# Kernel optimization log

Measured on AMD Instinct MI355X. Metric: run time of the kernel, lower is better.

Reference implementation:

```python
import jax, jax.numpy as jnp
import numpy as np

N, K, V_FEATS, FILTERS = 50000, 20, 128, 128


def setup_inputs() -> dict:
    key = jax.random.key(0)
    ks = jax.random.split(key, 10)
    vertices = jax.random.normal(ks[0], (N, V_FEATS), dtype=jnp.float32)
    nh_indices = jax.random.randint(ks[1], (N, K), -1, N, dtype=jnp.int32)
    int_indices = jax.random.randint(ks[2], (N, K), -1, N, dtype=jnp.int32)
    nh_edges = jax.random.uniform(ks[3], (N, K), dtype=jnp.float32)
    int_edges = jax.random.uniform(ks[4], (N, K), dtype=jnp.float32)
    is_int = jax.random.randint(ks[5], (N,), 0, 2, dtype=jnp.int32)
    scale = 1.0 / np.sqrt(V_FEATS)
    Wvc = jax.random.normal(ks[6], (V_FEATS, FILTERS), dtype=jnp.float32) * scale
    Wvn_int = jax.random.normal(ks[7], (V_FEATS, FILTERS), dtype=jnp.float32) * scale
    Wvn_nh = jax.random.normal(ks[8], (V_FEATS, FILTERS), dtype=jnp.float32) * scale
    bv = jnp.zeros((FILTERS,), dtype=jnp.float32)
    return {"vertices": vertices, "nh_indices": nh_indices, "int_indices": int_indices,
            "nh_edges": nh_edges, "int_edges": int_edges, "is_int": is_int,
            "Wvc": Wvc, "Wvn_int": Wvn_int, "Wvn_nh": Wvn_nh, "bv": bv}


def _gather_agg(v_proj, indices, edges):
    # v_proj: [N, F]; indices: [N, K] (-1 = pad); edges: [N, K]
    mask = (indices != -1)[..., None].astype(v_proj.dtype)            # [N, K, 1]
    norm = jnp.maximum(jnp.sum(indices > -1, axis=1, keepdims=True), 1).astype(v_proj.dtype)  # [N, 1]
    safe_idx = jnp.where(indices < 0, 0, indices)                      # masked slots -> dummy row 0
    gathered = v_proj[safe_idx]                                        # [N, K, F]
    return jnp.sum(gathered * mask * edges[..., None], axis=1) / norm  # [N, F]


def reference(vertices, nh_indices, int_indices, nh_edges, int_edges, is_int,
              Wvc, Wvn_int, Wvn_nh, bv):
    Zc = vertices @ Wvc                                # [N, F]
    v_Wvn_int = vertices @ Wvn_int                     # [N, F]
    v_Wvn_nh = vertices @ Wvn_nh                       # [N, F]
    Zn_inter = _gather_agg(v_Wvn_int, int_indices, int_edges)
    Zn_nh = _gather_agg(v_Wvn_nh, nh_indices, nh_edges)
    z = jax.nn.relu(Zc + Zn_inter + Zn_nh + bv)        # bias=True; dropout omitted (eval)
    return (z, nh_indices, int_indices, nh_edges, int_edges, is_int)
```

## Files before the change

### kernel.cpp

```cpp
#include <hip/hip_runtime.h>

#define N_VERT 50000
#define KNBR 20
#define F 128
#define NBLK 782

typedef unsigned int uint32;
typedef unsigned short ushort16;
typedef unsigned char uint8;
typedef __attribute__((ext_vector_type(8))) short bf16x8;
typedef __attribute__((ext_vector_type(4))) float f32x4;

__device__ __forceinline__ uint32 f2bf_bits(float x) {
    uint32 u = __float_as_uint(x);
    u += 0x7fff + ((u >> 16) & 1);
    return u >> 16;
}

__global__ __launch_bounds__(256) void wconv_kernel(
    const float* __restrict__ Wc, const float* __restrict__ Wi,
    const float* __restrict__ Wn, const float* __restrict__ bv,
    ushort16* __restrict__ Wt, float* __restrict__ bvp)
{
    int t = blockIdx.x * 256 + threadIdx.x;
    if (blockIdx.x == 0 && threadIdx.x < 128) {
        int c = threadIdx.x;
        bvp[c] = bv[(c & 7) * 16 + (c >> 3)];
    }
    if (t >= 3 * F * F) return;
    int w    = t >> 14;
    int r    = t & 16383;
    int kk   = r >> 12;
    int r2   = r & 4095;
    int nt   = r2 >> 9;
    int r3   = r2 & 511;
    int lane = r3 >> 3;
    int e    = r3 & 7;
    int k = kk * 32 + (lane >> 4) * 8 + e;
    int n = nt * 16 + (lane & 15);
    const float* W = (w == 0) ? Wc : ((w == 1) ? Wi : Wn);
    Wt[t] = (ushort16)f2bf_bits(W[k * F + n]);
}

__global__ __launch_bounds__(256) void mfma_proj_kernel(
    const float*    __restrict__ vert,
    const ushort16* __restrict__ Wt,
    const float*    __restrict__ bvp,
    ushort16* __restrict__ zcp,
    uint8* __restrict__ pay_i, float* __restrict__ sc_i,
    uint8* __restrict__ pay_n, float* __restrict__ sc_n)
{
    const int w    = blockIdx.y;
    const int wave = threadIdx.x >> 6;
    const int lane = threadIdx.x & 63;
    const int lr   = lane & 15;
    const int lk   = lane >> 4;
    const int rb   = (blockIdx.x * 4 + wave) * 16;

    int rowA = rb + lr; if (rowA > N_VERT - 1) rowA = N_VERT - 1;
    const float* vrow = vert + (size_t)rowA * F;
    bf16x8 afrag[4];
#pragma unroll
    for (int kk = 0; kk < 4; ++kk) {
        const float* p = vrow + kk * 32 + lk * 8;
        f32x4 lo = *(const f32x4*)p;
        f32x4 hi = *(const f32x4*)(p + 4);
#pragma unroll
        for (int j = 0; j < 4; ++j) {
            afrag[kk][j]     = (short)f2bf_bits(lo[j]);
            afrag[kk][4 + j] = (short)f2bf_bits(hi[j]);
        }
    }

    f32x4 acc[8];
#pragma unroll
    for (int nt = 0; nt < 8; ++nt) acc[nt] = (f32x4)(0.f);

#pragma unroll
    for (int kk = 0; kk < 4; ++kk)
#pragma unroll
        for (int nt = 0; nt < 8; ++nt) {
            bf16x8 b = *(const bf16x8*)(
                Wt + ((size_t)((w * 4 + kk) * 8 + nt)) * 512 + lane * 8);
            acc[nt] = __builtin_amdgcn_mfma_f32_16x16x32_bf16(
                afrag[kk], b, acc[nt], 0, 0, 0);
        }

    if (w == 0) {
        f32x4 bb0 = *(const f32x4*)(bvp + lr * 8);
        f32x4 bb1 = *(const f32x4*)(bvp + lr * 8 + 4);
        float bbv[8] = {bb0[0], bb0[1], bb0[2], bb0[3], bb1[0], bb1[1], bb1[2], bb1[3]};
#pragma unroll
        for (int j = 0; j < 4; ++j) {
            int row = rb + lk * 4 + j;
            uint32 d[4];
#pragma unroll
            for (int p = 0; p < 4; ++p)
                d[p] = f2bf_bits(acc[2 * p][j] + bbv[2 * p]) |
                       (f2bf_bits(acc[2 * p + 1][j] + bbv[2 * p + 1]) << 16);
            if (row < N_VERT)
                *(uint4*)((uint8*)zcp + (size_t)row * 256 + lr * 16) =
                    make_uint4(d[0], d[1], d[2], d[3]);
        }
    } else {
        uint8* pay = (w == 1) ? pay_i : pay_n;
        float* sc  = (w == 1) ? sc_i : sc_n;
        float m0 = 0.f, m1 = 0.f, m2 = 0.f, m3 = 0.f;
#pragma unroll
        for (int nt = 0; nt < 8; ++nt) {
            m0 = fmaxf(m0, fabsf(acc[nt][0]));
            m1 = fmaxf(m1, fabsf(acc[nt][1]));
            m2 = fmaxf(m2, fabsf(acc[nt][2]));
            m3 = fmaxf(m3, fabsf(acc[nt][3]));
        }
#pragma unroll
        for (int s = 1; s < 16; s <<= 1) {
            m0 = fmaxf(m0, __shfl_xor(m0, s));
            m1 = fmaxf(m1, __shfl_xor(m1, s));
            m2 = fmaxf(m2, __shfl_xor(m2, s));
            m3 = fmaxf(m3, __shfl_xor(m3, s));
        }
        float mj[4] = {m0, m1, m2, m3};
#pragma unroll
        for (int j = 0; j < 4; ++j) {
            int row = rb + lk * 4 + j;
            float inv = (mj[j] > 0.f) ? 127.f / mj[j] : 0.f;
            uint32 lo = 0, hi = 0;
#pragma unroll
            for (int nt = 0; nt < 4; ++nt) {
                int q0 = (int)rintf(acc[nt][j] * inv);
                int q1 = (int)rintf(acc[nt + 4][j] * inv);
                lo |= ((uint32)(q0 & 255)) << (8 * nt);
                hi |= ((uint32)(q1 & 255)) << (8 * nt);
            }
            if (row < N_VERT)
                *(uint2*)(pay + (size_t)row * 128 + lr * 8) = make_uint2(lo, hi);
        }
        float s_sel = (lr == 0) ? m0 : (lr == 1) ? m1 : (lr == 2) ? m2 : m3;
        if (lr < 4) {
            int row = rb + lk * 4 + lr;
            if (row < N_VERT) sc[row] = s_sel * (1.f / 127.f);
        }
    }
}

__global__ __launch_bounds__(256) void agg_kernel(
    const uint8*  __restrict__ pay_i, const float* __restrict__ sc_i,
    const uint8*  __restrict__ pay_n, const float* __restrict__ sc_n,
    const unsigned short* __restrict__ zcp,
    const int4*   __restrict__ int_idx4,
    const int4*   __restrict__ nh_idx4,
    const float4* __restrict__ int_e4,
    const float4* __restrict__ nh_e4,
    float* __restrict__ z)
{
    const int lane = threadIdx.x & 63;
    const int wave = threadIdx.x >> 6;
    const int vg   = lane >> 4;
    const int fg   = lane & 15;
    const int i    = blockIdx.x * 16 + wave * 4 + vg;

    float a_i[8], a_n[8];
#pragma unroll
    for (int j = 0; j < 8; ++j) { a_i[j] = 0.f; a_n[j] = 0.f; }
    int ci = 0, cn = 0;

    {
        int sidx[KNBR]; float f[KNBR];
#pragma unroll
        for (int q = 0; q < 5; ++q) {
            int4   a = int_idx4[i * 5 + q];
            float4 e = int_e4[i * 5 + q];
            int   av[4] = {a.x, a.y, a.z, a.w};
            float ev[4] = {e.x, e.y, e.z, e.w};
#pragma unroll
            for (int j = 0; j < 4; ++j) {
                bool v = av[j] >= 0;
                ci += v;
                sidx[4 * q + j] = v ? av[j] : 0;
                f[4 * q + j]    = v ? ev[j] : 0.f;
            }
        }
#pragma unroll
        for (int k = 0; k < KNBR; ++k) f[k] *= sc_i[sidx[k]];
        uint2 g[KNBR];
#pragma unroll
        for (int k = 0; k < KNBR; ++k)
            g[k] = *(const uint2*)(pay_i + (size_t)sidx[k] * 128 + fg * 8);
#pragma unroll
        for (int k = 0; k < KNBR; ++k) {
            float e = f[k];
            uint32 d0 = g[k].x, d1 = g[k].y;
#pragma unroll
            for (int b = 0; b < 4; ++b) {
                a_i[b]     = fmaf((float)((int)(d0 << (24 - 8 * b)) >> 24), e, a_i[b]);
                a_i[4 + b] = fmaf((float)((int)(d1 << (24 - 8 * b)) >> 24), e, a_i[4 + b]);
            }
        }
    }
    {
        int sidx[KNBR]; float f[KNBR];
#pragma unroll
        for (int q = 0; q < 5; ++q) {
            int4   a = nh_idx4[i * 5 + q];
            float4 e = nh_e4[i * 5 + q];
            int   av[4] = {a.x, a.y, a.z, a.w};
            float ev[4] = {e.x, e.y, e.z, e.w};
#pragma unroll
            for (int j = 0; j < 4; ++j) {
                bool v = av[j] >= 0;
                cn += v;
                sidx[4 * q + j] = v ? av[j] : 0;
                f[4 * q + j]    = v ? ev[j] : 0.f;
            }
        }
#pragma unroll
        for (int k = 0; k < KNBR; ++k) f[k] *= sc_n[sidx[k]];
        uint2 g[KNBR];
#pragma unroll
        for (int k = 0; k < KNBR; ++k)
            g[k] = *(const uint2*)(pay_n + (size_t)sidx[k] * 128 + fg * 8);
#pragma unroll
        for (int k = 0; k < KNBR; ++k) {
            float e = f[k];
            uint32 d0 = g[k].x, d1 = g[k].y;
#pragma unroll
            for (int b = 0; b < 4; ++b) {
                a_n[b]     = fmaf((float)((int)(d0 << (24 - 8 * b)) >> 24), e, a_n[b]);
                a_n[4 + b] = fmaf((float)((int)(d1 << (24 - 8 * b)) >> 24), e, a_n[4 + b]);
            }
        }
    }

    float ri = 1.f / (float)max(ci, 1);
    float rn = 1.f / (float)max(cn, 1);

    uint4 zq = *(const uint4*)(zcp + (size_t)i * 128 + fg * 8);
    uint32 zd[4] = {zq.x, zq.y, zq.z, zq.w};
    float* zrow = z + (size_t)i * F + fg;
#pragma unroll
    for (int t = 0; t < 8; ++t) {
        uint32 dw = zd[t >> 1];
        float zc = __uint_as_float((t & 1) ? (dw & 0xffff0000u) : (dw << 16));
        float r  = zc + a_i[t] * ri + a_n[t] * rn;
        zrow[t * 16] = fmaxf(r, 0.f);
    }
}

__global__ void pass_kernel(const int*   __restrict__ nh_idx,
                            const int*   __restrict__ int_idx,
                            const float* __restrict__ nh_e,
                            const float* __restrict__ int_e,
                            const int*   __restrict__ is_int,
                            float* __restrict__ out)
{
    const size_t NK    = (size_t)N_VERT * KNBR;
    const size_t total = 4 * NK + N_VERT;
    size_t t = (size_t)blockIdx.x * blockDim.x + threadIdx.x;
    if (t >= total) return;

    float v;
    if      (t <     NK) v = (float)nh_idx[t];
    else if (t < 2 * NK) v = (float)int_idx[t - NK];
    else if (t < 3 * NK) v = nh_e[t - 2 * NK];
    else if (t < 4 * NK) v = int_e[t - 3 * NK];
    else                 v = (float)is_int[t - 4 * NK];
    out[t] = v;
}

extern "C" void kernel_launch(void* const* d_in, const int* in_sizes, int n_in,
                              void* d_out, int out_size, void* d_ws, size_t ws_size,
                              hipStream_t stream) {
    const float* vert    = (const float*)d_in[0];
    const int*   nh_idx  = (const int*)  d_in[1];
    const int*   int_idx = (const int*)  d_in[2];
    const float* nh_e    = (const float*)d_in[3];
    const float* int_e   = (const float*)d_in[4];
    const int*   is_int  = (const int*)  d_in[5];
    const float* Wc      = (const float*)d_in[6];
    const float* Wi      = (const float*)d_in[7];
    const float* Wn      = (const float*)d_in[8];
    const float* bv      = (const float*)d_in[9];

    float* z        = (float*)d_out;
    float* out_rest = z + (size_t)N_VERT * F;

    uint8* pay_i = (uint8*)d_ws;
    uint8* pay_n = pay_i + (size_t)N_VERT * F;
    float* sc_i  = (float*)(pay_n + (size_t)N_VERT * F);
    float* sc_n  = sc_i + N_VERT;
    ushort16* zcp = (ushort16*)(sc_n + N_VERT);
    float* bvp   = (float*)(zcp + (size_t)N_VERT * F);
    ushort16* Wt = (ushort16*)(bvp + F);

    wconv_kernel<<<(3 * F * F + 255) / 256, 256, 0, stream>>>(Wc, Wi, Wn, bv, Wt, bvp);
    mfma_proj_kernel<<<dim3(NBLK, 3), 256, 0, stream>>>(
        vert, Wt, bvp, zcp, pay_i, sc_i, pay_n, sc_n);
    agg_kernel<<<N_VERT / 16, 256, 0, stream>>>(
        pay_i, sc_i, pay_n, sc_n, (const unsigned short*)zcp,
        (const int4*)int_idx, (const int4*)nh_idx,
        (const float4*)int_e, (const float4*)nh_e, z);

    const size_t total = (size_t)4 * N_VERT * KNBR + N_VERT;
    pass_kernel<<<(int)((total + 255) / 256), 256, 0, stream>>>(
        nh_idx, int_idx, nh_e, int_e, is_int, out_rest);
}
```

Measured before the change: 82.92 us.

## Fuse three projections per block and store neighbor payloads as FP8

The projection kernel now computes all three weight projections in one block, so each vertex row is read and converted to bf16 once instead of three times. The int8-with-per-row-scale payload is replaced by hardware FP8 pack/unpack conversions. This drops the max-reduction shuffles, the scale arrays and the per-neighbor scale gathers in the aggregation kernel. The cost is more accumulator registers (three sets of eight) in the projection kernel and lower precision, since FP8 without per-row scaling can lose accuracy or saturate on large values.

```diff
diff --git a/kernel.cpp b/kernel.cpp
--- a/kernel.cpp
+++ b/kernel.cpp
@@ -10,6 +10,7 @@
 typedef unsigned char uint8;
 typedef __attribute__((ext_vector_type(8))) short bf16x8;
 typedef __attribute__((ext_vector_type(4))) float f32x4;
+typedef __attribute__((ext_vector_type(2))) float f32x2;
 
 __device__ __forceinline__ uint32 f2bf_bits(float x) {
     uint32 u = __float_as_uint(x);
@@ -42,15 +43,14 @@
     Wt[t] = (ushort16)f2bf_bits(W[k * F + n]);
 }
 
-__global__ __launch_bounds__(256) void mfma_proj_kernel(
+__global__ __launch_bounds__(256, 3) void mfma_proj_kernel(
     const float*    __restrict__ vert,
     const ushort16* __restrict__ Wt,
     const float*    __restrict__ bvp,
     ushort16* __restrict__ zcp,
-    uint8* __restrict__ pay_i, float* __restrict__ sc_i,
-    uint8* __restrict__ pay_n, float* __restrict__ sc_n)
-{
-    const int w    = blockIdx.y;
+    uint8* __restrict__ pay_i,
+    uint8* __restrict__ pay_n)
+{
     const int wave = threadIdx.x >> 6;
     const int lane = threadIdx.x & 63;
     const int lr   = lane & 15;
@@ -72,81 +72,62 @@
         }
     }
 
-    f32x4 acc[8];
-#pragma unroll
-    for (int nt = 0; nt < 8; ++nt) acc[nt] = (f32x4)(0.f);
+    f32x4 aC[8], aI[8], aN[8];
+#pragma unroll
+    for (int nt = 0; nt < 8; ++nt) {
+        aC[nt] = (f32x4)(0.f); aI[nt] = (f32x4)(0.f); aN[nt] = (f32x4)(0.f);
+    }
 
 #pragma unroll
     for (int kk = 0; kk < 4; ++kk)
 #pragma unroll
         for (int nt = 0; nt < 8; ++nt) {
-            bf16x8 b = *(const bf16x8*)(
-                Wt + ((size_t)((w * 4 + kk) * 8 + nt)) * 512 + lane * 8);
-            acc[nt] = __builtin_amdgcn_mfma_f32_16x16x32_bf16(
-                afrag[kk], b, acc[nt], 0, 0, 0);
-        }
-
-    if (w == 0) {
-        f32x4 bb0 = *(const f32x4*)(bvp + lr * 8);
-        f32x4 bb1 = *(const f32x4*)(bvp + lr * 8 + 4);
-        float bbv[8] = {bb0[0], bb0[1], bb0[2], bb0[3], bb1[0], bb1[1], bb1[2], bb1[3]};
-#pragma unroll
-        for (int j = 0; j < 4; ++j) {
-            int row = rb + lk * 4 + j;
-            uint32 d[4];
-#pragma unroll
-            for (int p = 0; p < 4; ++p)
-                d[p] = f2bf_bits(acc[2 * p][j] + bbv[2 * p]) |
-                       (f2bf_bits(acc[2 * p + 1][j] + bbv[2 * p + 1]) << 16);
-            if (row < N_VERT)
-                *(uint4*)((uint8*)zcp + (size_t)row * 256 + lr * 16) =
-                    make_uint4(d[0], d[1], d[2], d[3]);
-        }
-    } else {
-        uint8* pay = (w == 1) ? pay_i : pay_n;
-        float* sc  = (w == 1) ? sc_i : sc_n;
-        float m0 = 0.f, m1 = 0.f, m2 = 0.f, m3 = 0.f;
-#pragma unroll
-        for (int nt = 0; nt < 8; ++nt) {
-            m0 = fmaxf(m0, fabsf(acc[nt][0]));
-            m1 = fmaxf(m1, fabsf(acc[nt][1]));
-            m2 = fmaxf(m2, fabsf(acc[nt][2]));
-            m3 = fmaxf(m3, fabsf(acc[nt][3]));
-        }
-#pragma unroll
-        for (int s = 1; s < 16; s <<= 1) {
-            m0 = fmaxf(m0, __shfl_xor(m0, s));
-            m1 = fmaxf(m1, __shfl_xor(m1, s));
-            m2 = fmaxf(m2, __shfl_xor(m2, s));
-            m3 = fmaxf(m3, __shfl_xor(m3, s));
-        }
-        float mj[4] = {m0, m1, m2, m3};
-#pragma unroll
-        for (int j = 0; j < 4; ++j) {
-            int row = rb + lk * 4 + j;
-            float inv = (mj[j] > 0.f) ? 127.f / mj[j] : 0.f;
-            uint32 lo = 0, hi = 0;
-#pragma unroll
-            for (int nt = 0; nt < 4; ++nt) {
-                int q0 = (int)rintf(acc[nt][j] * inv);
-                int q1 = (int)rintf(acc[nt + 4][j] * inv);
-                lo |= ((uint32)(q0 & 255)) << (8 * nt);
-                hi |= ((uint32)(q1 & 255)) << (8 * nt);
-            }
-            if (row < N_VERT)
-                *(uint2*)(pay + (size_t)row * 128 + lr * 8) = make_uint2(lo, hi);
-        }
-        float s_sel = (lr == 0) ? m0 : (lr == 1) ? m1 : (lr == 2) ? m2 : m3;
-        if (lr < 4) {
-            int row = rb + lk * 4 + lr;
-            if (row < N_VERT) sc[row] = s_sel * (1.f / 127.f);
-        }
+            const ushort16* base = Wt + (size_t)(kk * 8 + nt) * 512 + lane * 8;
+            bf16x8 bC = *(const bf16x8*)(base);
+            bf16x8 bI = *(const bf16x8*)(base + 32 * 512);
+            bf16x8 bN = *(const bf16x8*)(base + 64 * 512);
+            aC[nt] = __builtin_amdgcn_mfma_f32_16x16x32_bf16(afrag[kk], bC, aC[nt], 0, 0, 0);
+            aI[nt] = __builtin_amdgcn_mfma_f32_16x16x32_bf16(afrag[kk], bI, aI[nt], 0, 0, 0);
+            aN[nt] = __builtin_amdgcn_mfma_f32_16x16x32_bf16(afrag[kk], bN, aN[nt], 0, 0, 0);
+        }
+
+    f32x4 bb0 = *(const f32x4*)(bvp + lr * 8);
+    f32x4 bb1 = *(const f32x4*)(bvp + lr * 8 + 4);
+    float bbv[8] = {bb0[0], bb0[1], bb0[2], bb0[3], bb1[0], bb1[1], bb1[2], bb1[3]};
+#pragma unroll
+    for (int j = 0; j < 4; ++j) {
+        int row = rb + lk * 4 + j;
+        if (row >= N_VERT) continue;
+        uint32 d[4];
+#pragma unroll
+        for (int p = 0; p < 4; ++p)
+            d[p] = f2bf_bits(aC[2 * p][j] + bbv[2 * p]) |
+                   (f2bf_bits(aC[2 * p + 1][j] + bbv[2 * p + 1]) << 16);
+        *(uint4*)((uint8*)zcp + (size_t)row * 256 + lr * 16) =
+            make_uint4(d[0], d[1], d[2], d[3]);
+    }
+
+#pragma unroll
+    for (int j = 0; j < 4; ++j) {
+        int row = rb + lk * 4 + j;
+        if (row >= N_VERT) continue;
+        uint32 lo, hi;
+        lo = __builtin_amdgcn_cvt_pk_fp8_f32(aI[0][j], aI[1][j], 0, false);
+        lo = __builtin_amdgcn_cvt_pk_fp8_f32(aI[2][j], aI[3][j], lo, true);
+        hi = __builtin_amdgcn_cvt_pk_fp8_f32(aI[4][j], aI[5][j], 0, false);
+        hi = __builtin_amdgcn_cvt_pk_fp8_f32(aI[6][j], aI[7][j], hi, true);
+        *(uint2*)(pay_i + (size_t)row * 128 + lr * 8) = make_uint2(lo, hi);
+        lo = __builtin_amdgcn_cvt_pk_fp8_f32(aN[0][j], aN[1][j], 0, false);
+        lo = __builtin_amdgcn_cvt_pk_fp8_f32(aN[2][j], aN[3][j], lo, true);
+        hi = __builtin_amdgcn_cvt_pk_fp8_f32(aN[4][j], aN[5][j], 0, false);
+        hi = __builtin_amdgcn_cvt_pk_fp8_f32(aN[6][j], aN[7][j], hi, true);
+        *(uint2*)(pay_n + (size_t)row * 128 + lr * 8) = make_uint2(lo, hi);
     }
 }
 
 __global__ __launch_bounds__(256) void agg_kernel(
-    const uint8*  __restrict__ pay_i, const float* __restrict__ sc_i,
-    const uint8*  __restrict__ pay_n, const float* __restrict__ sc_n,
+    const uint8*  __restrict__ pay_i,
+    const uint8*  __restrict__ pay_n,
     const unsigned short* __restrict__ zcp,
     const int4*   __restrict__ int_idx4,
     const int4*   __restrict__ nh_idx4,
@@ -181,8 +162,6 @@
                 f[4 * q + j]    = v ? ev[j] : 0.f;
             }
         }
-#pragma unroll
-        for (int k = 0; k < KNBR; ++k) f[k] *= sc_i[sidx[k]];
         uint2 g[KNBR];
 #pragma unroll
         for (int k = 0; k < KNBR; ++k)
@@ -190,12 +169,18 @@
 #pragma unroll
         for (int k = 0; k < KNBR; ++k) {
             float e = f[k];
-            uint32 d0 = g[k].x, d1 = g[k].y;
-#pragma unroll
-            for (int b = 0; b < 4; ++b) {
-                a_i[b]     = fmaf((float)((int)(d0 << (24 - 8 * b)) >> 24), e, a_i[b]);
-                a_i[4 + b] = fmaf((float)((int)(d1 << (24 - 8 * b)) >> 24), e, a_i[4 + b]);
-            }
+            f32x2 p01 = __builtin_amdgcn_cvt_pk_f32_fp8((int)g[k].x, false);
+            f32x2 p23 = __builtin_amdgcn_cvt_pk_f32_fp8((int)g[k].x, true);
+            f32x2 p45 = __builtin_amdgcn_cvt_pk_f32_fp8((int)g[k].y, false);
+            f32x2 p67 = __builtin_amdgcn_cvt_pk_f32_fp8((int)g[k].y, true);
+            a_i[0] = fmaf(p01[0], e, a_i[0]);
+            a_i[1] = fmaf(p01[1], e, a_i[1]);
+            a_i[2] = fmaf(p23[0], e, a_i[2]);
+            a_i[3] = fmaf(p23[1], e, a_i[3]);
+            a_i[4] = fmaf(p45[0], e, a_i[4]);
+            a_i[5] = fmaf(p45[1], e, a_i[5]);
+            a_i[6] = fmaf(p67[0], e, a_i[6]);
+            a_i[7] = fmaf(p67[1], e, a_i[7]);
         }
     }
     {
@@ -214,8 +199,6 @@
                 f[4 * q + j]    = v ? ev[j] : 0.f;
             }
         }
-#pragma unroll
-        for (int k = 0; k < KNBR; ++k) f[k] *= sc_n[sidx[k]];
         uint2 g[KNBR];
 #pragma unroll
         for (int k = 0; k < KNBR; ++k)
@@ -223,12 +206,18 @@
 #pragma unroll
         for (int k = 0; k < KNBR; ++k) {
             float e = f[k];
-            uint32 d0 = g[k].x, d1 = g[k].y;
-#pragma unroll
-            for (int b = 0; b < 4; ++b) {
-                a_n[b]     = fmaf((float)((int)(d0 << (24 - 8 * b)) >> 24), e, a_n[b]);
-                a_n[4 + b] = fmaf((float)((int)(d1 << (24 - 8 * b)) >> 24), e, a_n[4 + b]);
-            }
+            f32x2 p01 = __builtin_amdgcn_cvt_pk_f32_fp8((int)g[k].x, false);
+            f32x2 p23 = __builtin_amdgcn_cvt_pk_f32_fp8((int)g[k].x, true);
+            f32x2 p45 = __builtin_amdgcn_cvt_pk_f32_fp8((int)g[k].y, false);
+            f32x2 p67 = __builtin_amdgcn_cvt_pk_f32_fp8((int)g[k].y, true);
+            a_n[0] = fmaf(p01[0], e, a_n[0]);
+            a_n[1] = fmaf(p01[1], e, a_n[1]);
+            a_n[2] = fmaf(p23[0], e, a_n[2]);
+            a_n[3] = fmaf(p23[1], e, a_n[3]);
+            a_n[4] = fmaf(p45[0], e, a_n[4]);
+            a_n[5] = fmaf(p45[1], e, a_n[5]);
+            a_n[6] = fmaf(p67[0], e, a_n[6]);
+            a_n[7] = fmaf(p67[1], e, a_n[7]);
         }
     }
 
@@ -287,17 +276,15 @@
 
     uint8* pay_i = (uint8*)d_ws;
     uint8* pay_n = pay_i + (size_t)N_VERT * F;
-    float* sc_i  = (float*)(pay_n + (size_t)N_VERT * F);
-    float* sc_n  = sc_i + N_VERT;
-    ushort16* zcp = (ushort16*)(sc_n + N_VERT);
+    ushort16* zcp = (ushort16*)(pay_n + (size_t)N_VERT * F);
     float* bvp   = (float*)(zcp + (size_t)N_VERT * F);
     ushort16* Wt = (ushort16*)(bvp + F);
 
     wconv_kernel<<<(3 * F * F + 255) / 256, 256, 0, stream>>>(Wc, Wi, Wn, bv, Wt, bvp);
-    mfma_proj_kernel<<<dim3(NBLK, 3), 256, 0, stream>>>(
-        vert, Wt, bvp, zcp, pay_i, sc_i, pay_n, sc_n);
+    mfma_proj_kernel<<<NBLK, 256, 0, stream>>>(
+        vert, Wt, bvp, zcp, pay_i, pay_n);
     agg_kernel<<<N_VERT / 16, 256, 0, stream>>>(
-        pay_i, sc_i, pay_n, sc_n, (const unsigned short*)zcp,
+        pay_i, pay_n, (const unsigned short*)zcp,
         (const int4*)int_idx, (const int4*)nh_idx,
         (const float4*)int_e, (const float4*)nh_e, z);
 
```

Measured after the change: 91.09 us. 9.9% more time.
